# Optimization experiments

Measured on AMD Instinct MI355X. Metric: run time of the kernel, lower is better.

Reference implementation:

```python
import jax, jax.numpy as jnp
import numpy as np

N = 50000          # nodes
E = 800000         # edges (avg degree 16)
F_IN = 64          # node feature dim
F_EDGE = 8         # edge feature dim (carried through, unused by EdgeConv)
DIMS = [64, 64, 64, 8]   # hidden layers + final num_classes layer (no BN)
EPS = 1e-5


def mish(x):
    return x * jnp.tanh(jax.nn.softplus(x))


def _init_layer(key, din, dout):
    k1, k2, k3, k4 = jax.random.split(key, 4)
    s1 = 1.0 / np.sqrt(2 * din)
    s2 = 1.0 / np.sqrt(dout)
    w1 = jax.random.uniform(k1, (2 * din, dout), jnp.float32, -s1, s1)
    b1 = jax.random.uniform(k2, (dout,), jnp.float32, -s1, s1)
    w2 = jax.random.uniform(k3, (dout, dout), jnp.float32, -s2, s2)
    b2 = jax.random.uniform(k4, (dout,), jnp.float32, -s2, s2)
    return w1, b1, w2, b2


def setup_inputs() -> dict:
    key = jax.random.key(0)
    ks = jax.random.split(key, 8)
    inp = {
        "x": jax.random.normal(ks[0], (N, F_IN), jnp.float32),
        "edge_index": jax.random.randint(ks[1], (2, E), 0, N, jnp.int32),
        "edge_attr": jax.random.normal(ks[2], (E, F_EDGE), jnp.float32),
    }
    din = F_IN
    for l, dout in enumerate(DIMS):
        w1, b1, w2, b2 = _init_layer(jax.random.fold_in(ks[3], l), din, dout)
        inp[f"w1_{l}"] = w1
        inp[f"b1_{l}"] = b1
        inp[f"w2_{l}"] = w2
        inp[f"b2_{l}"] = b2
        if l < len(DIMS) - 1:  # BN on all but final classifier layer
            inp[f"g_{l}"] = jnp.ones((dout,), jnp.float32)
            inp[f"be_{l}"] = jnp.zeros((dout,), jnp.float32)
        din = dout
    return inp


def _forward(x, edge_index, params):
    src = edge_index[0]
    dst = edge_index[1]
    for (w1, b1, w2, b2, g, be) in params:
        xi = x[dst]                       # [E, din] target feats
        xj = x[src]                       # [E, din] source feats
        m = jnp.concatenate([xi, xj - xi], axis=-1)   # [E, 2*din]
        h = mish(m @ w1 + b1) @ w2 + b2               # [E, dout]
        agg = jax.ops.segment_max(h, dst, num_segments=N)
        x = jnp.where(jnp.isfinite(agg), agg, 0.0)    # empty segments -> 0
        if g is not None:                 # BatchNorm1d, batch stats (train fwd)
            mu = x.mean(axis=0)
            var = x.var(axis=0)
            x = (x - mu) * jax.lax.rsqrt(var + EPS) * g + be
    return x


def reference(x, edge_index, edge_attr,
              w1_0, b1_0, w2_0, b2_0, g_0, be_0,
              w1_1, b1_1, w2_1, b2_1, g_1, be_1,
              w1_2, b1_2, w2_2, b2_2, g_2, be_2,
              w1_3, b1_3, w2_3, b2_3):
    params = [
        (w1_0, b1_0, w2_0, b2_0, g_0, be_0),
        (w1_1, b1_1, w2_1, b2_1, g_1, be_1),
        (w1_2, b1_2, w2_2, b2_2, g_2, be_2),
        (w1_3, b1_3, w2_3, b2_3, None, None),
    ]
    return _forward(x, edge_index, params)
```

## Files before the change

### kernel.cpp

```cpp
#include <hip/hip_runtime.h>
#include <hip/hip_bf16.h>
#include <math.h>

#define NN 50000
#define EE 800000
#define NT (EE / 16)
#define NTN (NN / 16)

#define NBLK64 1536
#define NW64 (NBLK64 * 4)
#define B64 (NT / NW64)
#define R64 (NT % NW64)

#define NBLK 1408
#define CHT 9

#define NBF 196
#define NWF (NBF * 4)

typedef short s8v __attribute__((ext_vector_type(8)));
typedef float f4v __attribute__((ext_vector_type(4)));

__device__ __forceinline__ short f2bf(float f) {
    unsigned u = __float_as_uint(f);
    u += 0x7fffu + ((u >> 16) & 1u);
    return (short)(u >> 16);
}

__device__ __forceinline__ unsigned enc(float f) {
    unsigned u = __float_as_uint(f);
    return (u & 0x80000000u) ? ~u : (u | 0x80000000u);
}
__device__ __forceinline__ float dec(unsigned k) {
    if (k == 0u) return 0.0f;
    unsigned u = (k & 0x80000000u) ? (k & 0x7fffffffu) : ~k;
    return __uint_as_float(u);
}

__device__ __forceinline__ float mish_fast(float v) {
    float t = __expf(v);
    float s = t * (t + 2.0f);
    float r = v * s * __builtin_amdgcn_rcpf(s + 2.0f);
    return (v > 15.0f) ? v : r;
}

#define MFMA16(a, b, c) __builtin_amdgcn_mfma_f32_16x16x32_bf16(a, b, c, 0, 0, 0)


__global__ __launch_bounds__(256) void count_k(const int* __restrict__ ei,
                                               int* __restrict__ cnt) {
    int e = blockIdx.x * 256 + threadIdx.x;
    if (e < EE) atomicAdd(&cnt[ei[EE + e]], 1);
}

#define NBS 196

__global__ __launch_bounds__(256) void scan_part(const int* __restrict__ cnt,
                                                 int* __restrict__ part) {
    int t = threadIdx.x, i = blockIdx.x * 256 + t;
    __shared__ int ps[256];
    ps[t] = (i < NN) ? cnt[i] : 0;
    __syncthreads();
    for (int off = 128; off > 0; off >>= 1) {
        if (t < off) ps[t] += ps[t + off];
        __syncthreads();
    }
    if (t == 0) part[blockIdx.x] = ps[0];
}

__global__ __launch_bounds__(256) void scan_top(int* __restrict__ part) {
    int t = threadIdx.x;
    int v = (t < NBS) ? part[t] : 0;
    __shared__ int ps[256];
    ps[t] = v;
    __syncthreads();
    for (int off = 1; off < 256; off <<= 1) {
        int u = (t >= off) ? ps[t - off] : 0;
        __syncthreads();
        ps[t] += u;
        __syncthreads();
    }
    if (t < NBS) part[t] = ps[t] - v;
}

__global__ __launch_bounds__(256) void scan_fin(const int* __restrict__ cnt,
                                                const int* __restrict__ part,
                                                int* __restrict__ row_off,
                                                int* __restrict__ cur) {
    int t = threadIdx.x, i = blockIdx.x * 256 + t;
    int v = (i < NN) ? cnt[i] : 0;
    __shared__ int ps[256];
    ps[t] = v;
    __syncthreads();
    for (int off = 1; off < 256; off <<= 1) {
        int u = (t >= off) ? ps[t - off] : 0;
        __syncthreads();
        ps[t] += u;
        __syncthreads();
    }
    int excl = ps[t] - v + part[blockIdx.x];
    if (i < NN) {
        row_off[i] = excl;
        cur[i] = excl;
        if (i == NN - 1) row_off[NN] = excl + v;
    }
}

__global__ __launch_bounds__(256) void scatter_k(const int* __restrict__ ei,
                                                 int* __restrict__ cur,
                                                 int* __restrict__ csr_src,
                                                 int* __restrict__ csr_dst) {
    int e = blockIdx.x * 256 + threadIdx.x;
    if (e < EE) {
        int d = ei[EE + e];
        int p = atomicAdd(&cur[d], 1);
        csr_src[p] = ei[e];
        csr_dst[p] = d;
    }
}


__global__ __launch_bounds__(256)
void cvt_a0(const float* __restrict__ x, const float* __restrict__ w1,
            const float* __restrict__ b1, unsigned short* __restrict__ xb,
            float* __restrict__ a0, unsigned* __restrict__ y,
            unsigned* __restrict__ y8) {
    const int tid = threadIdx.x;
    const int lane = tid & 63;
    const int wid = blockIdx.x * 4 + (tid >> 6);
    const int i = lane & 15, q = lane >> 4;
    s8v wf[4][2];
#pragma unroll
    for (int nb = 0; nb < 4; nb++)
#pragma unroll
        for (int kh = 0; kh < 2; kh++)
#pragma unroll
            for (int j = 0; j < 8; j++) {
                int k = kh * 32 + q * 8 + j, n = nb * 16 + i;
                wf[nb][kh][j] = f2bf(w1[k * 64 + n] - w1[(64 + k) * 64 + n]);
            }
    float bia[4];
#pragma unroll
    for (int nb = 0; nb < 4; nb++) bia[nb] = b1[nb * 16 + i];

    for (int t = wid; t < NTN; t += NWF) {
        const int row = t * 16 + i;
        const float* xr = x + (size_t)row * 64 + q * 8;
        f4v x0 = *(const f4v*)xr,        x1 = *(const f4v*)(xr + 4);
        f4v x2 = *(const f4v*)(xr + 32), x3 = *(const f4v*)(xr + 36);
        s8v af0, af1;
#pragma unroll
        for (int j = 0; j < 4; j++) {
            af0[j] = f2bf(x0[j]); af0[4 + j] = f2bf(x1[j]);
            af1[j] = f2bf(x2[j]); af1[4 + j] = f2bf(x3[j]);
        }
        unsigned short* xw = xb + (size_t)row * 64 + q * 8;
        *(s8v*)xw = af0;
        *(s8v*)(xw + 32) = af1;
        const int rowq = t * 16 + q * 4;
#pragma unroll
        for (int nb = 0; nb < 4; nb++) {
            f4v c = {0.f, 0.f, 0.f, 0.f};
            c = MFMA16(af0, wf[nb][0], c);
            c = MFMA16(af1, wf[nb][1], c);
#pragma unroll
            for (int r = 0; r < 4; r++)
                a0[(size_t)(rowq + r) * 64 + i * 4 + nb] = c[r] + bia[nb];
        }
    }
    const int gt = blockIdx.x * 256 + tid, gs = NBF * 256;
    for (int idx = gt; idx < NN * 64; idx += gs) y[idx] = 0u;
    for (int idx = gt; idx < NN * 8; idx += gs) y8[idx] = 0u;
}


__global__ __launch_bounds__(256)
void bn_a0_64(unsigned* __restrict__ yk, const float* __restrict__ st,
              const float* __restrict__ g, const float* __restrict__ be,
              const float* __restrict__ w1n, const float* __restrict__ b1n,
              unsigned short* __restrict__ xbout, float* __restrict__ a0out) {
    __shared__ float sa[64], sb[64];
    const int tid = threadIdx.x;
    if (tid < 64) {
        float mu  = st[tid] * (1.0f / NN);
        float var = st[64 + tid] * (1.0f / NN) - mu * mu;
        float sc  = rsqrtf(var + 1e-5f) * g[tid];
        sa[tid] = sc;
        sb[tid] = be[tid] - mu * sc;
    }
    __syncthreads();
    const int lane = tid & 63;
    const int wid = blockIdx.x * 4 + (tid >> 6);
    const int i = lane & 15, q = lane >> 4;

    s8v wf[4][2];
#pragma unroll
    for (int nb = 0; nb < 4; nb++)
#pragma unroll
        for (int kh = 0; kh < 2; kh++)
#pragma unroll
            for (int j = 0; j < 8; j++) {
                int k = kh * 32 + q * 8 + j, n = nb * 16 + i;
                wf[nb][kh][j] = f2bf(w1n[k * 64 + n] - w1n[(64 + k) * 64 + n]);
            }
    float bia[4];
#pragma unroll
    for (int nb = 0; nb < 4; nb++) bia[nb] = b1n[nb * 16 + i];

    f4v a00 = *(const f4v*)(sa + q * 8),      a01 = *(const f4v*)(sa + q * 8 + 4);
    f4v a10 = *(const f4v*)(sa + 32 + q * 8), a11 = *(const f4v*)(sa + 36 + q * 8);
    f4v b00 = *(const f4v*)(sb + q * 8),      b01 = *(const f4v*)(sb + q * 8 + 4);
    f4v b10 = *(const f4v*)(sb + 32 + q * 8), b11 = *(const f4v*)(sb + 36 + q * 8);

    const uint4 z4 = {0u, 0u, 0u, 0u};
    for (int t = wid; t < NTN; t += NWF) {
        const int row = t * 16 + i;
        unsigned* yr = yk + (size_t)row * 64 + q * 8;
        uint4 u0 = *(const uint4*)yr,        u1 = *(const uint4*)(yr + 4);
        uint4 u2 = *(const uint4*)(yr + 32), u3 = *(const uint4*)(yr + 36);
        s8v af0, af1;
        af0[0] = f2bf(dec(u0.x) * a00[0] + b00[0]);
        af0[1] = f2bf(dec(u0.y) * a00[1] + b00[1]);
        af0[2] = f2bf(dec(u0.z) * a00[2] + b00[2]);
        af0[3] = f2bf(dec(u0.w) * a00[3] + b00[3]);
        af0[4] = f2bf(dec(u1.x) * a01[0] + b01[0]);
        af0[5] = f2bf(dec(u1.y) * a01[1] + b01[1]);
        af0[6] = f2bf(dec(u1.z) * a01[2] + b01[2]);
        af0[7] = f2bf(dec(u1.w) * a01[3] + b01[3]);
        af1[0] = f2bf(dec(u2.x) * a10[0] + b10[0]);
        af1[1] = f2bf(dec(u2.y) * a10[1] + b10[1]);
        af1[2] = f2bf(dec(u2.z) * a10[2] + b10[2]);
        af1[3] = f2bf(dec(u2.w) * a10[3] + b10[3]);
        af1[4] = f2bf(dec(u3.x) * a11[0] + b11[0]);
        af1[5] = f2bf(dec(u3.y) * a11[1] + b11[1]);
        af1[6] = f2bf(dec(u3.z) * a11[2] + b11[2]);
        af1[7] = f2bf(dec(u3.w) * a11[3] + b11[3]);

        unsigned short* xw = xbout + (size_t)row * 64 + q * 8;
        *(s8v*)xw = af0;
        *(s8v*)(xw + 32) = af1;
        *(uint4*)yr = z4;        *(uint4*)(yr + 4) = z4;
        *(uint4*)(yr + 32) = z4; *(uint4*)(yr + 36) = z4;

        const int rowq = t * 16 + q * 4;
#pragma unroll
        for (int nb = 0; nb < 4; nb++) {
            f4v c = {0.f, 0.f, 0.f, 0.f};
            c = MFMA16(af0, wf[nb][0], c);
            c = MFMA16(af1, wf[nb][1], c);
#pragma unroll
            for (int r = 0; r < 4; r++)
                a0out[(size_t)(rowq + r) * 64 + i * 4 + nb] = c[r] + bia[nb];
        }
    }
}


__global__ __launch_bounds__(256)
void bn_a0_8(unsigned* __restrict__ yk, const float* __restrict__ st,
             const float* __restrict__ g, const float* __restrict__ be,
             const float* __restrict__ w1n, const float* __restrict__ b1n,
             unsigned short* __restrict__ xbout, float* __restrict__ a08) {
    __shared__ float sa[64], sb[64];
    const int tid = threadIdx.x;
    if (tid < 64) {
        float mu  = st[tid] * (1.0f / NN);
        float var = st[64 + tid] * (1.0f / NN) - mu * mu;
        float sc  = rsqrtf(var + 1e-5f) * g[tid];
        sa[tid] = sc;
        sb[tid] = be[tid] - mu * sc;
    }
    __syncthreads();
    const int lane = tid & 63;
    const int wid = blockIdx.x * 4 + (tid >> 6);
    const int i = lane & 15, q = lane >> 4;

    s8v wf[2];
#pragma unroll
    for (int kh = 0; kh < 2; kh++)
#pragma unroll
        for (int j = 0; j < 8; j++) {
            int k = kh * 32 + q * 8 + j;
            wf[kh][j] = (i < 8) ? f2bf(w1n[k * 8 + i] - w1n[(64 + k) * 8 + i]) : (short)0;
        }
    const float bia = (i < 8) ? b1n[i] : 0.0f;

    f4v a00 = *(const f4v*)(sa + q * 8),      a01 = *(const f4v*)(sa + q * 8 + 4);
    f4v a10 = *(const f4v*)(sa + 32 + q * 8), a11 = *(const f4v*)(sa + 36 + q * 8);
    f4v b00 = *(const f4v*)(sb + q * 8),      b01 = *(const f4v*)(sb + q * 8 + 4);
    f4v b10 = *(const f4v*)(sb + 32 + q * 8), b11 = *(const f4v*)(sb + 36 + q * 8);

    for (int t = wid; t < NTN; t += NWF) {
        const int row = t * 16 + i;
        const unsigned* yr = yk + (size_t)row * 64 + q * 8;
        uint4 u0 = *(const uint4*)yr,        u1 = *(const uint4*)(yr + 4);
        uint4 u2 = *(const uint4*)(yr + 32), u3 = *(const uint4*)(yr + 36);
        s8v af0, af1;
        af0[0] = f2bf(dec(u0.x) * a00[0] + b00[0]);
        af0[1] = f2bf(dec(u0.y) * a00[1] + b00[1]);
        af0[2] = f2bf(dec(u0.z) * a00[2] + b00[2]);
        af0[3] = f2bf(dec(u0.w) * a00[3] + b00[3]);
        af0[4] = f2bf(dec(u1.x) * a01[0] + b01[0]);
        af0[5] = f2bf(dec(u1.y) * a01[1] + b01[1]);
        af0[6] = f2bf(dec(u1.z) * a01[2] + b01[2]);
        af0[7] = f2bf(dec(u1.w) * a01[3] + b01[3]);
        af1[0] = f2bf(dec(u2.x) * a10[0] + b10[0]);
        af1[1] = f2bf(dec(u2.y) * a10[1] + b10[1]);
        af1[2] = f2bf(dec(u2.z) * a10[2] + b10[2]);
        af1[3] = f2bf(dec(u2.w) * a10[3] + b10[3]);
        af1[4] = f2bf(dec(u3.x) * a11[0] + b11[0]);
        af1[5] = f2bf(dec(u3.y) * a11[1] + b11[1]);
        af1[6] = f2bf(dec(u3.z) * a11[2] + b11[2]);
        af1[7] = f2bf(dec(u3.w) * a11[3] + b11[3]);

        unsigned short* xw = xbout + (size_t)row * 64 + q * 8;
        *(s8v*)xw = af0;
        *(s8v*)(xw + 32) = af1;

        f4v c = {0.f, 0.f, 0.f, 0.f};
        c = MFMA16(af0, wf[0], c);
        c = MFMA16(af1, wf[1], c);
        if (i < 8) {
            const int rowq = t * 16 + q * 4;
#pragma unroll
            for (int r = 0; r < 4; r++)
                a08[(size_t)(rowq + r) * 8 + i] = c[r] + bia;
        }
    }
}


__global__ __launch_bounds__(256)
void edge_mfma64(const unsigned short* __restrict__ xb, const float* __restrict__ a0,
                 const float* __restrict__ w1, const float* __restrict__ w2,
                 const float* __restrict__ b2,
                 const int* __restrict__ csr_src, const int* __restrict__ csr_dst,
                 unsigned* __restrict__ y) {
    __shared__ float uld[4][16 * 68];
    __shared__ int dseg[4][2][20];
    __shared__ short w2l[8 * 64 * 8];
    const int lane = threadIdx.x & 63;
    const int wv = threadIdx.x >> 6;
    const int wid = blockIdx.x * 4 + wv;
    const int i = lane & 15, q = lane >> 4;
    float* up = &uld[wv][0];

    s8v w1f[4][2];
#pragma unroll
    for (int nb = 0; nb < 4; nb++)
#pragma unroll
        for (int kh = 0; kh < 2; kh++)
#pragma unroll
            for (int j = 0; j < 8; j++) {
                int k = kh * 32 + q * 8 + j, n = nb * 16 + i;
                w1f[nb][kh][j] = f2bf(w1[(64 + k) * 64 + n]);
            }
    {
        const int nb = wv;
#pragma unroll
        for (int kh = 0; kh < 2; kh++) {
            s8v uu;
#pragma unroll
            for (int j = 0; j < 8; j++) {
                int k = kh * 32 + q * 8 + j;
                uu[j] = f2bf(w2[k * 64 + nb * 16 + i]);
            }
            *(s8v*)(w2l + ((nb * 2 + kh) * 64 + lane) * 8) = uu;
        }
    }
    __syncthreads();

    const float b2c = b2[lane];

    int t = wid * B64 + (wid < R64 ? wid : R64);
    const int tend = t + B64 + (wid < R64 ? 1 : 0);

    s8v af0_c, af1_c;
    {
        int s0 = csr_src[t * 16 + i];
        const unsigned short* xr = xb + (size_t)s0 * 64;
        af0_c = *(const s8v*)(xr + q * 8);
        af1_c = *(const s8v*)(xr + 32 + q * 8);
    }
    int src_n = (t + 1 < tend) ? csr_src[(t + 1) * 16 + i] : 0;
    if (lane < 17) {
        int e = t * 16 + lane;
        dseg[wv][t & 1][lane] = (e < EE) ? csr_dst[e] : -1;
    }
    asm volatile("s_waitcnt lgkmcnt(0)" ::: "memory");
    int dq_c[4];
#pragma unroll
    for (int r = 0; r < 4; r++) dq_c[r] = dseg[wv][t & 1][q * 4 + r];
    f4v a0r_c[4];
#pragma unroll
    for (int r = 0; r < 4; r++)
        a0r_c[r] = *(const f4v*)(a0 + (size_t)dq_c[r] * 64 + i * 4);

    float run = -INFINITY;

    for (; t < tend; t++) {
        const bool has_n = (t + 1) < tend;
        int* dsg = &dseg[wv][t & 1][0];
        int* dsg_n = &dseg[wv][(t + 1) & 1][0];

        if (has_n && lane < 17) {
            int e = (t + 1) * 16 + lane;
            dsg_n[lane] = (e < EE) ? csr_dst[e] : -1;
        }
        s8v af0_n = {0,0,0,0,0,0,0,0}, af1_n = {0,0,0,0,0,0,0,0};
        if (has_n) {
            const unsigned short* xr = xb + (size_t)src_n * 64;
            af0_n = *(const s8v*)(xr + q * 8);
            af1_n = *(const s8v*)(xr + 32 + q * 8);
        }
        int src_nn = (t + 2 < tend) ? csr_src[(t + 2) * 16 + i] : 0;

        f4v c0 = {0.f, 0.f, 0.f, 0.f}, c1 = c0, c2 = c0, c3 = c0;
        c0 = MFMA16(af0_c, w1f[0][0], c0); c0 = MFMA16(af1_c, w1f[0][1], c0);
        c1 = MFMA16(af0_c, w1f[1][0], c1); c1 = MFMA16(af1_c, w1f[1][1], c1);
        c2 = MFMA16(af0_c, w1f[2][0], c2); c2 = MFMA16(af1_c, w1f[2][1], c2);
        c3 = MFMA16(af0_c, w1f[3][0], c3); c3 = MFMA16(af1_c, w1f[3][1], c3);

        asm volatile("" ::: "memory");
#pragma unroll
        for (int r = 0; r < 4; r++) {
            const int ro = (q * 4 + r) * 68 + i;
            up[ro +  0] = mish_fast(c0[r] + a0r_c[r][0]);
            up[ro + 16] = mish_fast(c1[r] + a0r_c[r][1]);
            up[ro + 32] = mish_fast(c2[r] + a0r_c[r][2]);
            up[ro + 48] = mish_fast(c3[r] + a0r_c[r][3]);
        }
        asm volatile("s_waitcnt lgkmcnt(0)" ::: "memory");

        int dq_n[4];
        f4v a0r_n[4];
        if (has_n) {
#pragma unroll
            for (int r = 0; r < 4; r++) dq_n[r] = dsg_n[q * 4 + r];
#pragma unroll
            for (int r = 0; r < 4; r++)
                a0r_n[r] = *(const f4v*)(a0 + (size_t)dq_n[r] * 64 + i * 4);
        }

        s8v uf[2];
#pragma unroll
        for (int kh = 0; kh < 2; kh++) {
            const f4v* rp = (const f4v*)(up + i * 68 + kh * 32 + q * 8);
            f4v v0 = rp[0], v1 = rp[1];
            s8v uu;
            uu[0] = f2bf(v0[0]); uu[1] = f2bf(v0[1]);
            uu[2] = f2bf(v0[2]); uu[3] = f2bf(v0[3]);
            uu[4] = f2bf(v1[0]); uu[5] = f2bf(v1[1]);
            uu[6] = f2bf(v1[2]); uu[7] = f2bf(v1[3]);
            uf[kh] = uu;
        }
        asm volatile("" ::: "memory");

        f4v cc[4];
#pragma unroll
        for (int nb = 0; nb < 4; nb++) {
            s8v b0 = *(const s8v*)(w2l + ((nb * 2 + 0) * 64 + lane) * 8);
            s8v b1v = *(const s8v*)(w2l + ((nb * 2 + 1) * 64 + lane) * 8);
            f4v c = {0.f, 0.f, 0.f, 0.f};
            c = MFMA16(uf[0], b0, c);
            c = MFMA16(uf[1], b1v, c);
            cc[nb] = c;
        }

#pragma unroll
        for (int nb = 0; nb < 4; nb++)
#pragma unroll
            for (int r = 0; r < 4; r++)
                up[(q * 4 + r) * 68 + nb * 16 + i] = cc[nb][r];
        asm volatile("s_waitcnt lgkmcnt(0)" ::: "memory");

        float v[16];
#pragma unroll
        for (int row = 0; row < 16; row++) v[row] = up[row * 68 + lane];

        int dcur = dsg[0];
#pragma unroll
        for (int row = 0; row < 16; row++) {
            run = fmaxf(run, v[row]);
            int dn = (row < 15) ? dsg[row + 1] : (has_n ? dsg[16] : -1);
            if (dcur != dn) {
                atomicMax(&y[(size_t)dcur * 64 + lane], enc(run + b2c));
                run = -INFINITY;
            }
            dcur = dn;
        }
        asm volatile("s_waitcnt lgkmcnt(0)" ::: "memory");

        src_n = src_nn;
        af0_c = af0_n; af1_c = af1_n;
#pragma unroll
        for (int r = 0; r < 4; r++) a0r_c[r] = a0r_n[r];
    }
}


__global__ __launch_bounds__(256)
void edge_mfma16(const unsigned short* __restrict__ xb, const float* __restrict__ a0,
                 const float* __restrict__ w1, const float* __restrict__ w2,
                 const float* __restrict__ b2,
                 const int* __restrict__ csr_src, const int* __restrict__ csr_dst,
                 unsigned* __restrict__ y8) {
    __shared__ float uld[4][16 * 20];
    __shared__ int dseg[4][2][20];
    const int lane = threadIdx.x & 63;
    const int wv = threadIdx.x >> 6;
    const int wid = blockIdx.x * 4 + wv;
    const int i = lane & 15, q = lane >> 4;
    float* up = &uld[wv][0];

    s8v w1f[2], w2f;
#pragma unroll
    for (int kh = 0; kh < 2; kh++)
#pragma unroll
        for (int j = 0; j < 8; j++) {
            int k = kh * 32 + q * 8 + j;
            w1f[kh][j] = (i < 8) ? f2bf(w1[(64 + k) * 8 + i]) : (short)0;
        }
#pragma unroll
    for (int j = 0; j < 8; j++)
        w2f[j] = (q == 0 && i < 8) ? f2bf(w2[j * 8 + i]) : (short)0;
    const float b2c = (lane < 8) ? b2[lane] : 0.0f;

    int t = wid * CHT;
    if (t >= NT) return;
    const int tend = (t + CHT < NT) ? (t + CHT) : NT;

    s8v af0_c, af1_c;
    {
        int s0 = csr_src[t * 16 + i];
        const unsigned short* xr = xb + (size_t)s0 * 64;
        af0_c = *(const s8v*)(xr + q * 8);
        af1_c = *(const s8v*)(xr + 32 + q * 8);
    }
    int src_n = (t + 1 < tend) ? csr_src[(t + 1) * 16 + i] : 0;
    if (lane < 17) {
        int e = t * 16 + lane;
        dseg[wv][t & 1][lane] = (e < EE) ? csr_dst[e] : -1;
    }
    asm volatile("s_waitcnt lgkmcnt(0)" ::: "memory");
    int dq_c[4];
#pragma unroll
    for (int r = 0; r < 4; r++) dq_c[r] = dseg[wv][t & 1][q * 4 + r];
    float av_c[4];
#pragma unroll
    for (int r = 0; r < 4; r++)
        av_c[r] = (i < 8) ? a0[(size_t)dq_c[r] * 8 + i] : 0.0f;

    float run = -INFINITY;

    for (; t < tend; t++) {
        const bool has_n = (t + 1) < tend;
        int* dsg = &dseg[wv][t & 1][0];
        int* dsg_n = &dseg[wv][(t + 1) & 1][0];

        if (has_n && lane < 17) {
            int e = (t + 1) * 16 + lane;
            dsg_n[lane] = (e < EE) ? csr_dst[e] : -1;
        }
        s8v af0_n = {0,0,0,0,0,0,0,0}, af1_n = {0,0,0,0,0,0,0,0};
        if (has_n) {
            const unsigned short* xr = xb + (size_t)src_n * 64;
            af0_n = *(const s8v*)(xr + q * 8);
            af1_n = *(const s8v*)(xr + 32 + q * 8);
        }
        int src_nn = (t + 2 < tend) ? csr_src[(t + 2) * 16 + i] : 0;

        f4v c = {0.f, 0.f, 0.f, 0.f};
        c = MFMA16(af0_c, w1f[0], c);
        c = MFMA16(af1_c, w1f[1], c);

        asm volatile("" ::: "memory");
#pragma unroll
        for (int r = 0; r < 4; r++)
            up[(q * 4 + r) * 20 + i] = mish_fast(c[r] + av_c[r]);
        asm volatile("s_waitcnt lgkmcnt(0)" ::: "memory");

        int dq_n[4];
        float av_n[4] = {0, 0, 0, 0};
        if (has_n) {
#pragma unroll
            for (int r = 0; r < 4; r++) dq_n[r] = dsg_n[q * 4 + r];
#pragma unroll
            for (int r = 0; r < 4; r++)
                av_n[r] = (i < 8) ? a0[(size_t)dq_n[r] * 8 + i] : 0.0f;
        }

        s8v uf = {0,0,0,0,0,0,0,0};
        if (q < 2) {
            const f4v* rp = (const f4v*)(up + i * 20 + q * 8);
            f4v v0 = rp[0], v1 = rp[1];
            uf[0] = f2bf(v0[0]); uf[1] = f2bf(v0[1]);
            uf[2] = f2bf(v0[2]); uf[3] = f2bf(v0[3]);
            uf[4] = f2bf(v1[0]); uf[5] = f2bf(v1[1]);
            uf[6] = f2bf(v1[2]); uf[7] = f2bf(v1[3]);
        }
        asm volatile("" ::: "memory");

        f4v cc = {0.f, 0.f, 0.f, 0.f};
        cc = MFMA16(uf, w2f, cc);

#pragma unroll
        for (int r = 0; r < 4; r++)
            up[(q * 4 + r) * 20 + i] = cc[r];
        asm volatile("s_waitcnt lgkmcnt(0)" ::: "memory");

        float v[16];
#pragma unroll
        for (int row = 0; row < 16; row++) v[row] = up[row * 20 + (lane & 7)];

        int dcur = dsg[0];
#pragma unroll
        for (int row = 0; row < 16; row++) {
            run = fmaxf(run, v[row]);
            int dn = (row < 15) ? dsg[row + 1] : (has_n ? dsg[16] : -1);
            if (dcur != dn) {
                if (lane < 8)
                    atomicMax(&y8[(size_t)dcur * 8 + lane], enc(run + b2c));
                run = -INFINITY;
            }
            dcur = dn;
        }
        asm volatile("s_waitcnt lgkmcnt(0)" ::: "memory");

        src_n = src_nn;
        af0_c = af0_n; af1_c = af1_n;
#pragma unroll
        for (int r = 0; r < 4; r++) av_c[r] = av_n[r];
    }
}


__global__ __launch_bounds__(256)
void bn_stats(const unsigned* __restrict__ yk, float* __restrict__ st) {
    const int tid = threadIdx.x;
    const int ch = tid & 63, grp = tid >> 6;
    float s = 0, qq = 0;
    for (int n = blockIdx.x * 4 + grp; n < NN; n += gridDim.x * 4) {
        float v = dec(yk[(size_t)n * 64 + ch]);
        s += v;
        qq = fmaf(v, v, qq);
    }
    __shared__ float ls[256], lq[256];
    ls[tid] = s; lq[tid] = qq;
    __syncthreads();
    if (tid < 64) {
        s  = ls[tid] + ls[tid + 64] + ls[tid + 128] + ls[tid + 192];
        qq = lq[tid] + lq[tid + 64] + lq[tid + 128] + lq[tid + 192];
        atomicAdd(&st[ch], s);
        atomicAdd(&st[64 + ch], qq);
    }
}

__global__ __launch_bounds__(256)
void decode_out(const unsigned* __restrict__ y8, float* __restrict__ out) {
    int idx = blockIdx.x * 256 + threadIdx.x;
    if (idx < NN * 8) out[idx] = dec(y8[idx]);
}


extern "C" void kernel_launch(void* const* d_in, const int* in_sizes, int n_in,
                              void* d_out, int out_size, void* d_ws, size_t ws_size,
                              hipStream_t stream) {
    const float* x0 = (const float*)d_in[0];
    const int*   ei = (const int*)d_in[1];
    const float* w1[4] = {(const float*)d_in[3],  (const float*)d_in[9],
                          (const float*)d_in[15], (const float*)d_in[21]};
    const float* b1[4] = {(const float*)d_in[4],  (const float*)d_in[10],
                          (const float*)d_in[16], (const float*)d_in[22]};
    const float* w2[4] = {(const float*)d_in[5],  (const float*)d_in[11],
                          (const float*)d_in[17], (const float*)d_in[23]};
    const float* b2[4] = {(const float*)d_in[6],  (const float*)d_in[12],
                          (const float*)d_in[18], (const float*)d_in[24]};
    const float* gg[3] = {(const float*)d_in[7],  (const float*)d_in[13],
                          (const float*)d_in[19]};
    const float* be[3] = {(const float*)d_in[8],  (const float*)d_in[14],
                          (const float*)d_in[20]};

    char* p = (char*)d_ws;
    auto alloc = [&](size_t bytes) -> char* {
        char* r = p;
        p += (bytes + 255) & ~(size_t)255;
        return r;
    };
    int*      cnt     = (int*)alloc((size_t)NN * 4);
    int*      part    = (int*)alloc((size_t)NBS * 4);
    int*      row_off = (int*)alloc((size_t)(NN + 1) * 4);
    int*      cur     = (int*)alloc((size_t)NN * 4);
    int*      csr_s   = (int*)alloc((size_t)EE * 4);
    int*      csr_d   = (int*)alloc((size_t)EE * 4);
    float*    st      = (float*)alloc(3 * 128 * 4);
    float*    a0      = (float*)alloc((size_t)NN * 64 * 4);
    unsigned* y       = (unsigned*)alloc((size_t)NN * 64 * 4);
    unsigned* y8      = (unsigned*)alloc((size_t)NN * 8 * 4);
    unsigned short* xb0 = (unsigned short*)alloc((size_t)NN * 64 * 2);
    unsigned short* xbA = (unsigned short*)alloc((size_t)NN * 64 * 2);
    unsigned short* xbB = xb0;

    hipMemsetAsync(cnt, 0, (size_t)NN * 4, stream);
    hipMemsetAsync(st, 0, 3 * 128 * 4, stream);

    count_k<<<(EE + 255) / 256, 256, 0, stream>>>(ei, cnt);
    scan_part<<<NBS, 256, 0, stream>>>(cnt, part);
    scan_top<<<1, 256, 0, stream>>>(part);
    scan_fin<<<NBS, 256, 0, stream>>>(cnt, part, row_off, cur);
    scatter_k<<<(EE + 255) / 256, 256, 0, stream>>>(ei, cur, csr_s, csr_d);

    cvt_a0<<<NBF, 256, 0, stream>>>(x0, w1[0], b1[0], xb0, a0, y, y8);

    edge_mfma64<<<NBLK64, 256, 0, stream>>>(xb0, a0, w1[0], w2[0], b2[0],
                                            csr_s, csr_d, y);
    bn_stats<<<256, 256, 0, stream>>>(y, st);
    bn_a0_64<<<NBF, 256, 0, stream>>>(y, st, gg[0], be[0], w1[1], b1[1], xbA, a0);

    edge_mfma64<<<NBLK64, 256, 0, stream>>>(xbA, a0, w1[1], w2[1], b2[1],
                                            csr_s, csr_d, y);
    bn_stats<<<256, 256, 0, stream>>>(y, st + 128);
    bn_a0_64<<<NBF, 256, 0, stream>>>(y, st + 128, gg[1], be[1], w1[2], b1[2], xbB, a0);

    edge_mfma64<<<NBLK64, 256, 0, stream>>>(xbB, a0, w1[2], w2[2], b2[2],
                                            csr_s, csr_d, y);
    bn_stats<<<256, 256, 0, stream>>>(y, st + 256);
    bn_a0_8<<<NBF, 256, 0, stream>>>(y, st + 256, gg[2], be[2], w1[3], b1[3], xbA, a0);

    edge_mfma16<<<NBLK, 256, 0, stream>>>(xbA, a0, w1[3], w2[3], b2[3],
                                          csr_s, csr_d, y8);
    decode_out<<<(NN * 8 + 255) / 256, 256, 0, stream>>>(y8, (float*)d_out);
}
```

Before: 528.0 us.

## Pack mish output to bf16 in LDS and do segment-max in registers

The 64-wide edge kernel now writes the mish activations straight to shared memory as packed bf16 via v_cvt_pk_bf16_f32, and permutes the W2 layout so the A fragments for the second MFMA are loaded directly without per-element conversion. The segment-max is done first inside each lane's four MFMA rows, then over four per-quad partials staged through a small LDS buffer. This drops the full 16x64 fp32 LDS round trip and the 16-row serial scan. The running max no longer carries across tiles, so each tile issues at least one atomicMax per segment piece, which adds atomic traffic. The block count is also raised from 1536 to 1792.

```diff
diff --git a/kernel.cpp b/kernel.cpp
--- a/kernel.cpp
+++ b/kernel.cpp
@@ -7,7 +7,7 @@
 #define NT (EE / 16)
 #define NTN (NN / 16)
 
-#define NBLK64 1536
+#define NBLK64 1792
 #define NW64 (NBLK64 * 4)
 #define B64 (NT / NW64)
 #define R64 (NT % NW64)
@@ -25,6 +25,12 @@
     unsigned u = __float_as_uint(f);
     u += 0x7fffu + ((u >> 16) & 1u);
     return (short)(u >> 16);
+}
+
+__device__ __forceinline__ unsigned cvtpk(float lo, float hi) {
+    unsigned r;
+    asm("v_cvt_pk_bf16_f32 %0, %1, %2" : "=v"(r) : "v"(lo), "v"(hi));
+    return r;
 }
 
 __device__ __forceinline__ unsigned enc(float f) {
@@ -336,14 +342,16 @@
                  const float* __restrict__ b2,
                  const int* __restrict__ csr_src, const int* __restrict__ csr_dst,
                  unsigned* __restrict__ y) {
-    __shared__ float uld[4][16 * 68];
-    __shared__ int dseg[4][2][20];
+    __shared__ __align__(16) unsigned short uld[4][16 * 72];
+    __shared__ float spar[4][4 * 68];
+    __shared__ int dseg[4][2][16];
     __shared__ short w2l[8 * 64 * 8];
     const int lane = threadIdx.x & 63;
     const int wv = threadIdx.x >> 6;
     const int wid = blockIdx.x * 4 + wv;
     const int i = lane & 15, q = lane >> 4;
-    float* up = &uld[wv][0];
+    unsigned short* up = &uld[wv][0];
+    float* spw = &spar[wv][0];
 
     s8v w1f[4][2];
 #pragma unroll
@@ -356,21 +364,23 @@
                 w1f[nb][kh][j] = f2bf(w1[(64 + k) * 64 + n]);
             }
     {
-        const int nb = wv;
+        const int nbo = wv;
 #pragma unroll
         for (int kh = 0; kh < 2; kh++) {
             s8v uu;
 #pragma unroll
             for (int j = 0; j < 8; j++) {
-                int k = kh * 32 + q * 8 + j;
-                uu[j] = f2bf(w2[k * 64 + nb * 16 + i]);
+                int ch = 16 * (j & 3) + 2 * q + 8 * kh + (j >> 2);
+                uu[j] = f2bf(w2[ch * 64 + nbo * 16 + i]);
             }
-            *(s8v*)(w2l + ((nb * 2 + kh) * 64 + lane) * 8) = uu;
+            *(s8v*)(w2l + ((nbo * 2 + kh) * 64 + lane) * 8) = uu;
         }
     }
     __syncthreads();
 
-    const float b2c = b2[lane];
+    const float b2s = b2[lane];
+    const float b2n0 = b2[i],      b2n1 = b2[16 + i];
+    const float b2n2 = b2[32 + i], b2n3 = b2[48 + i];
 
     int t = wid * B64 + (wid < R64 ? wid : R64);
     const int tend = t + B64 + (wid < R64 ? 1 : 0);
@@ -383,10 +393,7 @@
         af1_c = *(const s8v*)(xr + 32 + q * 8);
     }
     int src_n = (t + 1 < tend) ? csr_src[(t + 1) * 16 + i] : 0;
-    if (lane < 17) {
-        int e = t * 16 + lane;
-        dseg[wv][t & 1][lane] = (e < EE) ? csr_dst[e] : -1;
-    }
+    if (lane < 16) dseg[wv][t & 1][lane] = csr_dst[t * 16 + lane];
     asm volatile("s_waitcnt lgkmcnt(0)" ::: "memory");
     int dq_c[4];
 #pragma unroll
@@ -396,17 +403,13 @@
     for (int r = 0; r < 4; r++)
         a0r_c[r] = *(const f4v*)(a0 + (size_t)dq_c[r] * 64 + i * 4);
 
-    float run = -INFINITY;
-
     for (; t < tend; t++) {
         const bool has_n = (t + 1) < tend;
-        int* dsg = &dseg[wv][t & 1][0];
+        const int* dsg = &dseg[wv][t & 1][0];
         int* dsg_n = &dseg[wv][(t + 1) & 1][0];
 
-        if (has_n && lane < 17) {
-            int e = (t + 1) * 16 + lane;
-            dsg_n[lane] = (e < EE) ? csr_dst[e] : -1;
-        }
+        if (has_n && lane < 16) dsg_n[lane] = csr_dst[(t + 1) * 16 + lane];
+
         s8v af0_n = {0,0,0,0,0,0,0,0}, af1_n = {0,0,0,0,0,0,0,0};
         if (has_n) {
             const unsigned short* xr = xb + (size_t)src_n * 64;
@@ -424,11 +427,14 @@
         asm volatile("" ::: "memory");
 #pragma unroll
         for (int r = 0; r < 4; r++) {
-            const int ro = (q * 4 + r) * 68 + i;
-            up[ro +  0] = mish_fast(c0[r] + a0r_c[r][0]);
-            up[ro + 16] = mish_fast(c1[r] + a0r_c[r][1]);
-            up[ro + 32] = mish_fast(c2[r] + a0r_c[r][2]);
-            up[ro + 48] = mish_fast(c3[r] + a0r_c[r][3]);
+            float m0 = mish_fast(c0[r] + a0r_c[r][0]);
+            float m1v = mish_fast(c1[r] + a0r_c[r][1]);
+            float m2v = mish_fast(c2[r] + a0r_c[r][2]);
+            float m3v = mish_fast(c3[r] + a0r_c[r][3]);
+            uint2 pw;
+            pw.x = cvtpk(m0, m1v);
+            pw.y = cvtpk(m2v, m3v);
+            *(uint2*)(up + (q * 4 + r) * 72 + 4 * i) = pw;
         }
         asm volatile("s_waitcnt lgkmcnt(0)" ::: "memory");
 
@@ -442,59 +448,78 @@
                 a0r_n[r] = *(const f4v*)(a0 + (size_t)dq_n[r] * 64 + i * 4);
         }
 
-        s8v uf[2];
-#pragma unroll
-        for (int kh = 0; kh < 2; kh++) {
-            const f4v* rp = (const f4v*)(up + i * 68 + kh * 32 + q * 8);
-            f4v v0 = rp[0], v1 = rp[1];
-            s8v uu;
-            uu[0] = f2bf(v0[0]); uu[1] = f2bf(v0[1]);
-            uu[2] = f2bf(v0[2]); uu[3] = f2bf(v0[3]);
-            uu[4] = f2bf(v1[0]); uu[5] = f2bf(v1[1]);
-            uu[6] = f2bf(v1[2]); uu[7] = f2bf(v1[3]);
-            uf[kh] = uu;
-        }
+        s8v uf0 = *(const s8v*)(up + i * 72 + q * 8);
+        s8v uf1 = *(const s8v*)(up + i * 72 + (q + 4) * 8);
         asm volatile("" ::: "memory");
 
         f4v cc[4];
 #pragma unroll
         for (int nb = 0; nb < 4; nb++) {
-            s8v b0 = *(const s8v*)(w2l + ((nb * 2 + 0) * 64 + lane) * 8);
-            s8v b1v = *(const s8v*)(w2l + ((nb * 2 + 1) * 64 + lane) * 8);
+            s8v bb0 = *(const s8v*)(w2l + ((nb * 2 + 0) * 64 + lane) * 8);
+            s8v bb1 = *(const s8v*)(w2l + ((nb * 2 + 1) * 64 + lane) * 8);
             f4v c = {0.f, 0.f, 0.f, 0.f};
-            c = MFMA16(uf[0], b0, c);
-            c = MFMA16(uf[1], b1v, c);
+            c = MFMA16(uf0, bb0, c);
+            c = MFMA16(uf1, bb1, c);
             cc[nb] = c;
         }
 
-#pragma unroll
-        for (int nb = 0; nb < 4; nb++)
-#pragma unroll
-            for (int r = 0; r < 4; r++)
-                up[(q * 4 + r) * 68 + nb * 16 + i] = cc[nb][r];
+        float r0 = cc[0][0], r1 = cc[1][0], r2 = cc[2][0], r3 = cc[3][0];
+
+#define SCAN_STEP(RR)                                                        \
+        {                                                                    \
+            bool mm = (dq_c[RR] != dq_c[RR - 1]);                            \
+            if (__any(mm)) {                                                 \
+                if (mm) {                                                    \
+                    size_t bse = (size_t)dq_c[RR - 1] * 64 + i;              \
+                    atomicMax(&y[bse],      enc(r0 + b2n0));                 \
+                    atomicMax(&y[bse + 16], enc(r1 + b2n1));                 \
+                    atomicMax(&y[bse + 32], enc(r2 + b2n2));                 \
+                    atomicMax(&y[bse + 48], enc(r3 + b2n3));                 \
+                }                                                            \
+                r0 = mm ? cc[0][RR] : fmaxf(r0, cc[0][RR]);                  \
+                r1 = mm ? cc[1][RR] : fmaxf(r1, cc[1][RR]);                  \
+                r2 = mm ? cc[2][RR] : fmaxf(r2, cc[2][RR]);                  \
+                r3 = mm ? cc[3][RR] : fmaxf(r3, cc[3][RR]);                  \
+            } else {                                                         \
+                r0 = fmaxf(r0, cc[0][RR]); r1 = fmaxf(r1, cc[1][RR]);        \
+                r2 = fmaxf(r2, cc[2][RR]); r3 = fmaxf(r3, cc[3][RR]);        \
+            }                                                                \
+        }
+        SCAN_STEP(1)
+        SCAN_STEP(2)
+        SCAN_STEP(3)
+#undef SCAN_STEP
+
+        spw[q * 68 +       i] = r0;
+        spw[q * 68 + 16 +  i] = r1;
+        spw[q * 68 + 32 +  i] = r2;
+        spw[q * 68 + 48 +  i] = r3;
         asm volatile("s_waitcnt lgkmcnt(0)" ::: "memory");
 
-        float v[16];
-#pragma unroll
-        for (int row = 0; row < 16; row++) v[row] = up[row * 68 + lane];
-
-        int dcur = dsg[0];
-#pragma unroll
-        for (int row = 0; row < 16; row++) {
-            run = fmaxf(run, v[row]);
-            int dn = (row < 15) ? dsg[row + 1] : (has_n ? dsg[16] : -1);
-            if (dcur != dn) {
-                atomicMax(&y[(size_t)dcur * 64 + lane], enc(run + b2c));
-                run = -INFINITY;
-            }
-            dcur = dn;
-        }
+        float v0 = spw[lane],       v1 = spw[68 + lane];
+        float v2s = spw[136 + lane], v3s = spw[204 + lane];
+        int e0 = dsg[3], e1 = dsg[7], e2 = dsg[11], e3 = dsg[15];
+
+        float run2 = v0; int dc = e0;
+        if (e1 != dc) {
+            atomicMax(&y[(size_t)dc * 64 + lane], enc(run2 + b2s));
+            run2 = v1; dc = e1;
+        } else run2 = fmaxf(run2, v1);
+        if (e2 != dc) {
+            atomicMax(&y[(size_t)dc * 64 + lane], enc(run2 + b2s));
+            run2 = v2s; dc = e2;
+        } else run2 = fmaxf(run2, v2s);
+        if (e3 != dc) {
+            atomicMax(&y[(size_t)dc * 64 + lane], enc(run2 + b2s));
+            run2 = v3s; dc = e3;
+        } else run2 = fmaxf(run2, v3s);
+        atomicMax(&y[(size_t)dc * 64 + lane], enc(run2 + b2s));
         asm volatile("s_waitcnt lgkmcnt(0)" ::: "memory");
 
         src_n = src_nn;
         af0_c = af0_n; af1_c = af1_n;
 #pragma unroll
-        for (int r = 0; r < 4; r++) a0r_c[r] = a0r_n[r];
+        for (int r = 0; r < 4; r++) { dq_c[r] = dq_n[r]; a0r_c[r] = a0r_n[r]; }
     }
 }
 
```

New measurement: 512.0 us. 3.0% less time.
